# Kernel optimization log

Measured on AMD Instinct MI355X. Metric: run time of the kernel, lower is better.

Reference implementation:

```python
import jax, jax.numpy as jnp
import numpy as np
import math

NUM_HEADS = 8
HEAD_SIZE = 32

def get_alibi_slopes(n_heads):
    def pow2_slopes(n):
        start = 2.0 ** (-2.0 ** (-(math.log2(n) - 3)))
        ratio = start
        return [start * ratio ** i for i in range(n)]
    if math.log2(n_heads).is_integer():
        return np.array(pow2_slopes(n_heads), dtype=np.float32)
    cp2 = 2 ** math.floor(math.log2(n_heads))
    extra = pow2_slopes(2 * cp2)[0::2][: n_heads - cp2]
    return np.array(pow2_slopes(cp2) + extra, dtype=np.float32)

ALIBI_SLOPES = jnp.asarray(get_alibi_slopes(NUM_HEADS))  # [H]

def setup_inputs() -> dict:
    key = jax.random.key(0)
    ks = jax.random.split(key, 6)
    B, T, C = 32, 512, 256
    s = 1.0 / math.sqrt(C)
    return {
        "x": jax.random.normal(ks[0], (B, T, C), dtype=jnp.float32),
        "Wq": jax.random.normal(ks[1], (C, NUM_HEADS * HEAD_SIZE), dtype=jnp.float32) * s,
        "Wk": jax.random.normal(ks[2], (C, NUM_HEADS * HEAD_SIZE), dtype=jnp.float32) * s,
        "Wv": jax.random.normal(ks[3], (C, NUM_HEADS * HEAD_SIZE), dtype=jnp.float32) * s,
        "Wo": jax.random.normal(ks[4], (NUM_HEADS * HEAD_SIZE, C), dtype=jnp.float32) * s,
        "bo": jax.random.normal(ks[5], (C,), dtype=jnp.float32) * 0.01,
    }

def reference(x, Wq, Wk, Wv, Wo, bo):
    # Faithful eval-mode forward (dropout disabled) of the torch MultiHeadAttention.
    B, T, C = x.shape
    H, D = NUM_HEADS, HEAD_SIZE
    q = (x @ Wq).reshape(B, T, H, D).transpose(0, 2, 1, 3)  # [B,H,T,D]
    k = (x @ Wk).reshape(B, T, H, D).transpose(0, 2, 1, 3)
    v = (x @ Wv).reshape(B, T, H, D).transpose(0, 2, 1, 3)
    scale = 1.0 / math.sqrt(D)
    wei = jnp.einsum("bhtd,bhsd->bhts", q, k) * scale  # [B,H,T,T]
    pos = jnp.arange(T)
    rel = (pos[None, :] - pos[:, None]).astype(jnp.float32)  # bias[i,j] = j - i
    bias = ALIBI_SLOPES[:, None, None] * rel[None, :, :]      # [H,T,T]
    wei = wei + bias[None]
    causal = pos[None, :] <= pos[:, None]  # [T,T], True where j <= i
    wei = jnp.where(causal[None, None], wei, -jnp.inf)
    wei = jax.nn.softmax(wei, axis=-1)
    out = jnp.einsum("bhts,bhsd->bhtd", wei, v)  # [B,H,T,D]
    out = out.transpose(0, 2, 1, 3).reshape(B, T, H * D)
    return out @ Wo + bo
```

## Files before the change

kernel.cpp:

```cpp
#include <hip/hip_runtime.h>
#include <stdint.h>

#define LOG2E 1.4426950408889634f

typedef __attribute__((ext_vector_type(8))) short bf16x8;
typedef __attribute__((ext_vector_type(4))) float f32x4;

__device__ __forceinline__ unsigned short f2bf(float f) {
  union { float f; unsigned int u; } v; v.f = f;
  unsigned int u = v.u;
  u += 0x7FFFu + ((u >> 16) & 1u);
  return (unsigned short)(u >> 16);
}

__device__ __forceinline__ unsigned int cvt_pk_bf16(float lo, float hi) {
  unsigned int r;
  asm("v_cvt_pk_bf16_f32 %0, %1, %2" : "=v"(r) : "v"(lo), "v"(hi));
  return r;
}

struct WPtrs { const float* src[4]; unsigned short* dst[4]; };
__global__ void transpose_w(WPtrs p) {
  __shared__ float tile[32][33];
  const float* src = p.src[blockIdx.z];
  unsigned short* dst = p.dst[blockIdx.z];
  int x = blockIdx.x * 32 + threadIdx.x;
  int y = blockIdx.y * 32 + threadIdx.y;
  #pragma unroll
  for (int j = 0; j < 32; j += 8)
    tile[threadIdx.y + j][threadIdx.x] = src[(y + j) * 256 + x];
  __syncthreads();
  int xo = blockIdx.y * 32 + threadIdx.x;
  int yo = blockIdx.x * 32 + threadIdx.y;
  #pragma unroll
  for (int j = 0; j < 32; j += 8)
    dst[(yo + j) * 256 + xo] = f2bf(tile[threadIdx.x][threadIdx.y + j]);
}

__launch_bounds__(256, 3)
__global__ void gemm_qkv(const float* __restrict__ Ax,
                         const unsigned short* __restrict__ Wt,
                         unsigned short* __restrict__ q_out,
                         unsigned short* __restrict__ k_out,
                         unsigned short* __restrict__ vT) {
  __shared__ unsigned short As[64][72];
  __shared__ unsigned short Bs[256][72];
  const int tid = threadIdx.x;
  const int m0 = blockIdx.x * 64;
  const int wsel = blockIdx.y;
  const unsigned short* W = Wt + wsel * 65536;
  const int w = tid >> 6, lane = tid & 63;
  const int n0 = w * 64;
  const int lr = lane & 15, lg = lane >> 4;

  f32x4 acc[4][4] = {};

  for (int kt = 0; kt < 4; ++kt) {
    #pragma unroll
    for (int i = 0; i < 2; ++i) {
      int c = tid + i * 256;
      int row = c >> 3, colg = c & 7;
      const float* s = &Ax[(size_t)(m0 + row) * 256 + kt * 64 + colg * 8];
      float4 f0 = *reinterpret_cast<const float4*>(s);
      float4 f1 = *reinterpret_cast<const float4*>(s + 4);
      uint4 pk;
      pk.x = cvt_pk_bf16(f0.x, f0.y); pk.y = cvt_pk_bf16(f0.z, f0.w);
      pk.z = cvt_pk_bf16(f1.x, f1.y); pk.w = cvt_pk_bf16(f1.z, f1.w);
      *reinterpret_cast<uint4*>(&As[row][colg * 8]) = pk;
    }
    #pragma unroll
    for (int i = 0; i < 8; ++i) {
      int c = tid + i * 256;
      int row = c >> 3, colg = c & 7;
      *reinterpret_cast<int4*>(&Bs[row][colg * 8]) =
        *reinterpret_cast<const int4*>(&W[(size_t)row * 256 + kt * 64 + colg * 8]);
    }
    __syncthreads();
    #pragma unroll
    for (int kk = 0; kk < 2; ++kk) {
      bf16x8 af[4], bfr[4];
      #pragma unroll
      for (int mf = 0; mf < 4; ++mf)
        af[mf] = *reinterpret_cast<const bf16x8*>(&As[mf * 16 + lr][kk * 32 + lg * 8]);
      #pragma unroll
      for (int nf = 0; nf < 4; ++nf)
        bfr[nf] = *reinterpret_cast<const bf16x8*>(&Bs[n0 + nf * 16 + lr][kk * 32 + lg * 8]);
      #pragma unroll
      for (int mf = 0; mf < 4; ++mf)
        #pragma unroll
        for (int nf = 0; nf < 4; ++nf)
          acc[mf][nf] = __builtin_amdgcn_mfma_f32_16x16x32_bf16(af[mf], bfr[nf], acc[mf][nf], 0, 0, 0);
    }
    __syncthreads();
  }

  if (wsel < 2) {
    unsigned short* dst = (wsel == 0) ? q_out : k_out;
    #pragma unroll
    for (int mf = 0; mf < 4; ++mf)
      #pragma unroll
      for (int nf = 0; nf < 4; ++nf)
        #pragma unroll
        for (int r = 0; r < 4; ++r)
          dst[(size_t)(m0 + mf * 16 + lg * 4 + r) * 256 + (n0 + nf * 16 + lr)] =
            f2bf(acc[mf][nf][r]);
  } else {
    #pragma unroll
    for (int mf = 0; mf < 4; ++mf)
      #pragma unroll
      for (int nf = 0; nf < 4; ++nf) {
        int ncol = n0 + nf * 16 + lr;
        int h = ncol >> 5, d = ncol & 31;
        int m = m0 + mf * 16 + lg * 4;
        int b = m >> 9, t = m & 511;
        ushort4 pk;
        pk.x = f2bf(acc[mf][nf][0]); pk.y = f2bf(acc[mf][nf][1]);
        pk.z = f2bf(acc[mf][nf][2]); pk.w = f2bf(acc[mf][nf][3]);
        *reinterpret_cast<ushort4*>(&vT[((size_t)((b * 8 + h) * 32 + d)) * 512 + t]) = pk;
      }
  }
}

__launch_bounds__(256, 3)
__global__ void gemm_out(const unsigned short* __restrict__ Ab,
                         const unsigned short* __restrict__ W,
                         const float* __restrict__ bo,
                         float* __restrict__ f_out) {
  __shared__ unsigned short As[128][72];
  __shared__ unsigned short Bs[128][72];
  const int tid = threadIdx.x;
  const int m0 = blockIdx.x * 128;
  const int n0 = blockIdx.y * 128;
  const int w = tid >> 6, lane = tid & 63;
  const int wm = (w >> 1) * 64, wn = (w & 1) * 64;
  const int lr = lane & 15, lg = lane >> 4;

  f32x4 acc[4][4] = {};

  for (int kt = 0; kt < 4; ++kt) {
    #pragma unroll
    for (int cc = 0; cc < 4; ++cc) {
      int c = tid + cc * 256;
      int row = c >> 3, colg = c & 7;
      *reinterpret_cast<int4*>(&As[row][colg * 8]) =
        *reinterpret_cast<const int4*>(&Ab[(size_t)(m0 + row) * 256 + kt * 64 + colg * 8]);
      *reinterpret_cast<int4*>(&Bs[row][colg * 8]) =
        *reinterpret_cast<const int4*>(&W[(size_t)(n0 + row) * 256 + kt * 64 + colg * 8]);
    }
    __syncthreads();
    #pragma unroll
    for (int kk = 0; kk < 2; ++kk) {
      bf16x8 af[4], bfr[4];
      #pragma unroll
      for (int mf = 0; mf < 4; ++mf)
        af[mf] = *reinterpret_cast<const bf16x8*>(&As[wm + mf * 16 + lr][kk * 32 + lg * 8]);
      #pragma unroll
      for (int nf = 0; nf < 4; ++nf)
        bfr[nf] = *reinterpret_cast<const bf16x8*>(&Bs[wn + nf * 16 + lr][kk * 32 + lg * 8]);
      #pragma unroll
      for (int mf = 0; mf < 4; ++mf)
        #pragma unroll
        for (int nf = 0; nf < 4; ++nf)
          acc[mf][nf] = __builtin_amdgcn_mfma_f32_16x16x32_bf16(af[mf], bfr[nf], acc[mf][nf], 0, 0, 0);
    }
    __syncthreads();
  }

  #pragma unroll
  for (int mf = 0; mf < 4; ++mf)
    #pragma unroll
    for (int nf = 0; nf < 4; ++nf)
      #pragma unroll
      for (int r = 0; r < 4; ++r) {
        int ncol = n0 + wn + nf * 16 + lr;
        f_out[(size_t)(m0 + wm + mf * 16 + lg * 4 + r) * 256 + ncol] = acc[mf][nf][r] + bo[ncol];
      }
}

struct CSt {
  bf16x8 qf;
  f32x4 o0, o1;
  float m, l, bb0;
  int nfull, qq;
};

__device__ __forceinline__ void attn_init(CSt& st, int c, const unsigned short* qb,
    int b, int h, int lr, int lg, float slope2) {
  st.qq = c * 16;
  st.qf = *reinterpret_cast<const bf16x8*>(
      &qb[(size_t)(b * 512 + st.qq + lr) * 256 + h * 32 + lg * 8]);
  f32x4 z = {0.f, 0.f, 0.f, 0.f};
  st.o0 = z; st.o1 = z;
  st.m = -1e30f; st.l = 0.f;
  st.nfull = (st.qq >= 63) ? ((st.qq - 63) / 64 + 1) : 0;
  st.bb0 = slope2 * (float)(lg * 4 - lr - st.qq);
}

__device__ __forceinline__ void attn_step(CSt& st, int s,
    const bf16x8* kf, const bf16x8* vf, char* __restrict__ Pw,
    int lr, int lg, float scale2, float slope2, const float* cc, int swz) {
  const int kb0 = s * 64;
  f32x4 sv[4];
  #pragma unroll
  for (int t = 0; t < 4; ++t) {
    f32x4 z = {0.f, 0.f, 0.f, 0.f};
    sv[t] = __builtin_amdgcn_mfma_f32_16x16x32_bf16(kf[t], st.qf, z, 0, 0, 0);
  }
  float bb = st.bb0 + slope2 * (float)kb0;
  float x[16];
  #pragma unroll
  for (int t = 0; t < 4; ++t)
    #pragma unroll
    for (int r = 0; r < 4; ++r)
      x[t * 4 + r] = sv[t][r] * scale2 + (bb + cc[t * 4 + r]);
  if (s >= st.nfull) {
    int thr = st.qq + lr - kb0 - lg * 4;
    #pragma unroll
    for (int t = 0; t < 4; ++t)
      #pragma unroll
      for (int r = 0; r < 4; ++r)
        x[t * 4 + r] = ((t * 16 + r) <= thr) ? x[t * 4 + r] : -1e30f;
  }
  float bm = x[0];
  #pragma unroll
  for (int j = 1; j < 16; ++j) bm = fmaxf(bm, x[j]);
  bm = fmaxf(bm, __shfl_xor(bm, 16));
  bm = fmaxf(bm, __shfl_xor(bm, 32));
  float mn = fmaxf(st.m, bm);
  float alpha = __builtin_amdgcn_exp2f(st.m - mn);
  st.m = mn;
  st.l *= alpha;
  #pragma unroll
  for (int r = 0; r < 4; ++r) { st.o0[r] *= alpha; st.o1[r] *= alpha; }
  float ps = 0.f;
  #pragma unroll
  for (int j = 0; j < 16; ++j) { x[j] = __builtin_amdgcn_exp2f(x[j] - mn); ps += x[j]; }
  st.l += ps;
  char* Prow = Pw + lr * 128;
  #pragma unroll
  for (int t = 0; t < 4; ++t)
    #pragma unroll
    for (int pp = 0; pp < 2; ++pp) {
      unsigned int w2 = cvt_pk_bf16(x[t * 4 + 2 * pp], x[t * 4 + 2 * pp + 1]);
      *reinterpret_cast<unsigned int*>(Prow + ((t * 32 + lg * 8 + pp * 4) ^ swz)) = w2;
    }
  #pragma unroll
  for (int ks = 0; ks < 2; ++ks) {
    bf16x8 pb = *reinterpret_cast<const bf16x8*>(Prow + ((ks * 64 + lg * 16) ^ swz));
    st.o0 = __builtin_amdgcn_mfma_f32_16x16x32_bf16(vf[ks * 2 + 0], pb, st.o0, 0, 0, 0);
    st.o1 = __builtin_amdgcn_mfma_f32_16x16x32_bf16(vf[ks * 2 + 1], pb, st.o1, 0, 0, 0);
  }
}

__device__ __forceinline__ void attn_fin(CSt& st, unsigned short* __restrict__ ob,
                                         int b, int h, int lr, int lg) {
  float l = st.l;
  l += __shfl_xor(l, 16);
  l += __shfl_xor(l, 32);
  float inv = 1.0f / l;
  unsigned int w0 = cvt_pk_bf16(st.o0[0] * inv, st.o0[1] * inv);
  unsigned int w1 = cvt_pk_bf16(st.o0[2] * inv, st.o0[3] * inv);
  unsigned int w2 = cvt_pk_bf16(st.o1[0] * inv, st.o1[1] * inv);
  unsigned int w3 = cvt_pk_bf16(st.o1[2] * inv, st.o1[3] * inv);
  size_t obase = (size_t)(b * 512 + st.qq + lr) * 256 + h * 32;
  *reinterpret_cast<uint2*>(&ob[obase + lg * 4]) = make_uint2(w0, w1);
  *reinterpret_cast<uint2*>(&ob[obase + 16 + lg * 4]) = make_uint2(w2, w3);
}

__launch_bounds__(256, 2)
__global__ void attn_k(const unsigned short* __restrict__ qb,
                       const unsigned short* __restrict__ kb,
                       const unsigned short* __restrict__ vT,
                       unsigned short* __restrict__ ob) {
  __shared__ unsigned short Ks[512 * 32];
  __shared__ unsigned short Vs[32 * 512];
  __shared__ char Pb[16384];
  const int p = blockIdx.x, h = blockIdx.y, b = blockIdx.z;
  const int tid = threadIdx.x, wv = tid >> 6, lane = tid & 63;
  const int lr = lane & 15, lg = lane >> 4;

  {
    const unsigned short* ksrc = kb + ((size_t)b * 512) * 256 + h * 32;
    #pragma unroll
    for (int it = 0; it < 8; ++it) {
      int idx = tid + it * 256;
      int row = idx >> 2, g = idx & 3;
      int gs = g ^ ((row >> 1) & 3);
      *reinterpret_cast<int4*>(&Ks[row * 32 + gs * 8]) =
        *reinterpret_cast<const int4*>(&ksrc[(size_t)row * 256 + g * 8]);
    }
    const unsigned short* vsrc = vT + ((size_t)(b * 8 + h) * 32) * 512;
    #pragma unroll
    for (int it = 0; it < 8; ++it) {
      int idx = tid + it * 256;
      int d = idx >> 6, cg = idx & 63;
      int col = (cg * 8) ^ ((d & 7) << 3);
      *reinterpret_cast<int4*>(&Vs[d * 512 + col]) =
        *reinterpret_cast<const int4*>(&vsrc[(size_t)d * 512 + cg * 8]);
    }
  }
  __syncthreads();

  const float scale2 = 0.17677669529663687f * LOG2E;
  const float slope2 = exp2f(-(float)(h + 1)) * LOG2E;
  float cc[16];
  #pragma unroll
  for (int t = 0; t < 4; ++t)
    #pragma unroll
    for (int r = 0; r < 4; ++r) cc[t * 4 + r] = slope2 * (float)(t * 16 + r);
  const int swz = (lr & 7) << 4;
  const int kchunk = (lg ^ ((lr >> 1) & 3)) * 8;
  char* Pw0 = Pb + wv * 4096;
  char* Pw1 = Pw0 + 2048;

  const int g = p * 4 + wv;
  const int c0 = g, c1 = 15 - g, c2 = 16 + g, c3 = 31 - g;
  CSt s0, s1, s2, s3;
  attn_init(s0, c0, qb, b, h, lr, lg, slope2);
  attn_init(s1, c1, qb, b, h, lr, lg, slope2);
  attn_init(s2, c2, qb, b, h, lr, lg, slope2);
  attn_init(s3, c3, qb, b, h, lr, lg, slope2);
  const int n0 = c0 / 4 + 1, n1 = c1 / 4 + 1, n2 = c2 / 4 + 1, n3 = c3 / 4 + 1;

  for (int s = 0; s < n3; ++s) {
    const int kb0 = s * 64;
    bf16x8 kf[4], vf[4];
    #pragma unroll
    for (int t = 0; t < 4; ++t)
      kf[t] = *reinterpret_cast<const bf16x8*>(&Ks[(kb0 + t * 16 + lr) * 32 + kchunk]);
    #pragma unroll
    for (int ks = 0; ks < 2; ++ks)
      #pragma unroll
      for (int dt = 0; dt < 2; ++dt) {
        int d = dt * 16 + lr;
        int col = (kb0 + ks * 32 + lg * 8) ^ ((d & 7) << 3);
        vf[ks * 2 + dt] = *reinterpret_cast<const bf16x8*>(&Vs[d * 512 + col]);
      }
    if (s < n0) attn_step(s0, s, kf, vf, Pw0, lr, lg, scale2, slope2, cc, swz);
    if (s < n1) attn_step(s1, s, kf, vf, Pw1, lr, lg, scale2, slope2, cc, swz);
    if (s < n2) attn_step(s2, s, kf, vf, Pw0, lr, lg, scale2, slope2, cc, swz);
    attn_step(s3, s, kf, vf, Pw1, lr, lg, scale2, slope2, cc, swz);
  }

  attn_fin(s0, ob, b, h, lr, lg);
  attn_fin(s1, ob, b, h, lr, lg);
  attn_fin(s2, ob, b, h, lr, lg);
  attn_fin(s3, ob, b, h, lr, lg);
}

extern "C" void kernel_launch(void* const* d_in, const int* in_sizes, int n_in,
                              void* d_out, int out_size, void* d_ws, size_t ws_size,
                              hipStream_t stream) {
  const float* x  = (const float*)d_in[0];
  const float* Wq = (const float*)d_in[1];
  const float* Wk = (const float*)d_in[2];
  const float* Wv = (const float*)d_in[3];
  const float* Wo = (const float*)d_in[4];
  const float* bo = (const float*)d_in[5];
  float* out = (float*)d_out;

  char* ws = (char*)d_ws;
  unsigned short* qb = (unsigned short*)(ws);
  unsigned short* kb = (unsigned short*)(ws + (8u  << 20));
  unsigned short* vT = (unsigned short*)(ws + (16u << 20));
  unsigned short* ob = (unsigned short*)(ws + (24u << 20));
  unsigned short* wt = (unsigned short*)(ws + (32u << 20));

  WPtrs p;
  p.src[0] = Wq; p.src[1] = Wk; p.src[2] = Wv; p.src[3] = Wo;
  p.dst[0] = wt; p.dst[1] = wt + 65536; p.dst[2] = wt + 2 * 65536; p.dst[3] = wt + 3 * 65536;
  transpose_w<<<dim3(8, 8, 4), dim3(32, 8), 0, stream>>>(p);

  gemm_qkv<<<dim3(256, 3), 256, 0, stream>>>(x, wt, qb, kb, vT);
  attn_k<<<dim3(2, 8, 32), 256, 0, stream>>>(qb, kb, vT, ob);
  gemm_out<<<dim3(128, 2), 256, 0, stream>>>(ob, wt + 3 * 65536, bo, out);
}
```

Measured before the change: 58.70 us.

## Drop LDS staging in attention, read K/V from global and shuffle P in registers

The attention kernel stops staging K and V for the whole head in shared memory and instead loads the MFMA fragments straight from global memory (L2/L1-cached) on each step. The P tile is no longer written to and read back from LDS; packed bf16 values are moved between lanes with wave shuffles to form the MFMA B operand. Each wave now handles two balanced query chunks instead of four, the grid doubles, and launch bounds target 3 blocks per SM. This removes the upfront LDS fill, the block barrier and the LDS round-trip for P, at the cost of redundant global reads of K/V across blocks, uncoalesced strided fragment loads, and extra shuffle instructions.

```diff
diff --git a/kernel.cpp b/kernel.cpp
--- a/kernel.cpp
+++ b/kernel.cpp
@@ -197,8 +197,8 @@
 }
 
 __device__ __forceinline__ void attn_step(CSt& st, int s,
-    const bf16x8* kf, const bf16x8* vf, char* __restrict__ Pw,
-    int lr, int lg, float scale2, float slope2, const float* cc, int swz) {
+    const bf16x8* kf, const bf16x8* vf,
+    int lr, int lg, float scale2, float slope2, const float* cc) {
   const int kb0 = s * 64;
   f32x4 sv[4];
   #pragma unroll
@@ -236,19 +236,30 @@
   #pragma unroll
   for (int j = 0; j < 16; ++j) { x[j] = __builtin_amdgcn_exp2f(x[j] - mn); ps += x[j]; }
   st.l += ps;
-  char* Prow = Pw + lr * 128;
+  unsigned int wpk[4][2];
   #pragma unroll
   for (int t = 0; t < 4; ++t)
     #pragma unroll
-    for (int pp = 0; pp < 2; ++pp) {
-      unsigned int w2 = cvt_pk_bf16(x[t * 4 + 2 * pp], x[t * 4 + 2 * pp + 1]);
-      *reinterpret_cast<unsigned int*>(Prow + ((t * 32 + lg * 8 + pp * 4) ^ swz)) = w2;
-    }
+    for (int pp = 0; pp < 2; ++pp)
+      wpk[t][pp] = cvt_pk_bf16(x[t * 4 + 2 * pp], x[t * 4 + 2 * pp + 1]);
+  const int src0 = lr + (((lg & 1) * 2) << 4);
+  const int src1 = src0 + 16;
+  const bool hi = (lg >> 1) != 0;
   #pragma unroll
   for (int ks = 0; ks < 2; ++ks) {
-    bf16x8 pb = *reinterpret_cast<const bf16x8*>(Prow + ((ks * 64 + lg * 16) ^ swz));
-    st.o0 = __builtin_amdgcn_mfma_f32_16x16x32_bf16(vf[ks * 2 + 0], pb, st.o0, 0, 0, 0);
-    st.o1 = __builtin_amdgcn_mfma_f32_16x16x32_bf16(vf[ks * 2 + 1], pb, st.o1, 0, 0, 0);
+    unsigned long long Ap = ((unsigned long long)wpk[2 * ks + 1][0] << 32) | wpk[2 * ks][0];
+    unsigned long long Bp = ((unsigned long long)wpk[2 * ks + 1][1] << 32) | wpk[2 * ks][1];
+    unsigned long long A0 = (unsigned long long)__shfl((long long)Ap, src0, 64);
+    unsigned long long B0 = (unsigned long long)__shfl((long long)Bp, src0, 64);
+    unsigned long long A1 = (unsigned long long)__shfl((long long)Ap, src1, 64);
+    unsigned long long B1 = (unsigned long long)__shfl((long long)Bp, src1, 64);
+    union { uint4 u; bf16x8 v; } pb;
+    pb.u.x = hi ? (unsigned int)(A0 >> 32) : (unsigned int)A0;
+    pb.u.y = hi ? (unsigned int)(B0 >> 32) : (unsigned int)B0;
+    pb.u.z = hi ? (unsigned int)(A1 >> 32) : (unsigned int)A1;
+    pb.u.w = hi ? (unsigned int)(B1 >> 32) : (unsigned int)B1;
+    st.o0 = __builtin_amdgcn_mfma_f32_16x16x32_bf16(vf[ks * 2 + 0], pb.v, st.o0, 0, 0, 0);
+    st.o1 = __builtin_amdgcn_mfma_f32_16x16x32_bf16(vf[ks * 2 + 1], pb.v, st.o1, 0, 0, 0);
   }
 }
 
@@ -267,39 +278,14 @@
   *reinterpret_cast<uint2*>(&ob[obase + 16 + lg * 4]) = make_uint2(w2, w3);
 }
 
-__launch_bounds__(256, 2)
+__launch_bounds__(256, 3)
 __global__ void attn_k(const unsigned short* __restrict__ qb,
                        const unsigned short* __restrict__ kb,
                        const unsigned short* __restrict__ vT,
                        unsigned short* __restrict__ ob) {
-  __shared__ unsigned short Ks[512 * 32];
-  __shared__ unsigned short Vs[32 * 512];
-  __shared__ char Pb[16384];
-  const int p = blockIdx.x, h = blockIdx.y, b = blockIdx.z;
+  const int h = blockIdx.y, b = blockIdx.z;
   const int tid = threadIdx.x, wv = tid >> 6, lane = tid & 63;
   const int lr = lane & 15, lg = lane >> 4;
-
-  {
-    const unsigned short* ksrc = kb + ((size_t)b * 512) * 256 + h * 32;
-    #pragma unroll
-    for (int it = 0; it < 8; ++it) {
-      int idx = tid + it * 256;
-      int row = idx >> 2, g = idx & 3;
-      int gs = g ^ ((row >> 1) & 3);
-      *reinterpret_cast<int4*>(&Ks[row * 32 + gs * 8]) =
-        *reinterpret_cast<const int4*>(&ksrc[(size_t)row * 256 + g * 8]);
-    }
-    const unsigned short* vsrc = vT + ((size_t)(b * 8 + h) * 32) * 512;
-    #pragma unroll
-    for (int it = 0; it < 8; ++it) {
-      int idx = tid + it * 256;
-      int d = idx >> 6, cg = idx & 63;
-      int col = (cg * 8) ^ ((d & 7) << 3);
-      *reinterpret_cast<int4*>(&Vs[d * 512 + col]) =
-        *reinterpret_cast<const int4*>(&vsrc[(size_t)d * 512 + cg * 8]);
-    }
-  }
-  __syncthreads();
 
   const float scale2 = 0.17677669529663687f * LOG2E;
   const float slope2 = exp2f(-(float)(h + 1)) * LOG2E;
@@ -308,44 +294,36 @@
   for (int t = 0; t < 4; ++t)
     #pragma unroll
     for (int r = 0; r < 4; ++r) cc[t * 4 + r] = slope2 * (float)(t * 16 + r);
-  const int swz = (lr & 7) << 4;
-  const int kchunk = (lg ^ ((lr >> 1) & 3)) * 8;
-  char* Pw0 = Pb + wv * 4096;
-  char* Pw1 = Pw0 + 2048;
-
-  const int g = p * 4 + wv;
-  const int c0 = g, c1 = 15 - g, c2 = 16 + g, c3 = 31 - g;
-  CSt s0, s1, s2, s3;
-  attn_init(s0, c0, qb, b, h, lr, lg, slope2);
-  attn_init(s1, c1, qb, b, h, lr, lg, slope2);
-  attn_init(s2, c2, qb, b, h, lr, lg, slope2);
-  attn_init(s3, c3, qb, b, h, lr, lg, slope2);
-  const int n0 = c0 / 4 + 1, n1 = c1 / 4 + 1, n2 = c2 / 4 + 1, n3 = c3 / 4 + 1;
-
-  for (int s = 0; s < n3; ++s) {
+
+  const int j = blockIdx.x * 4 + wv;
+  const int cA = j, cB = 31 - j;
+  CSt A, B;
+  attn_init(A, cA, qb, b, h, lr, lg, slope2);
+  attn_init(B, cB, qb, b, h, lr, lg, slope2);
+  const int nA = cA / 4 + 1, nB = cB / 4 + 1;
+
+  const unsigned short* kbase = kb + ((size_t)b * 512) * 256 + h * 32;
+  const unsigned short* vbase = vT + ((size_t)(b * 8 + h) * 32) * 512;
+
+  for (int s = 0; s < nB; ++s) {
     const int kb0 = s * 64;
     bf16x8 kf[4], vf[4];
     #pragma unroll
     for (int t = 0; t < 4; ++t)
-      kf[t] = *reinterpret_cast<const bf16x8*>(&Ks[(kb0 + t * 16 + lr) * 32 + kchunk]);
+      kf[t] = *reinterpret_cast<const bf16x8*>(
+          &kbase[(size_t)(kb0 + t * 16 + lr) * 256 + lg * 8]);
     #pragma unroll
     for (int ks = 0; ks < 2; ++ks)
       #pragma unroll
-      for (int dt = 0; dt < 2; ++dt) {
-        int d = dt * 16 + lr;
-        int col = (kb0 + ks * 32 + lg * 8) ^ ((d & 7) << 3);
-        vf[ks * 2 + dt] = *reinterpret_cast<const bf16x8*>(&Vs[d * 512 + col]);
-      }
-    if (s < n0) attn_step(s0, s, kf, vf, Pw0, lr, lg, scale2, slope2, cc, swz);
-    if (s < n1) attn_step(s1, s, kf, vf, Pw1, lr, lg, scale2, slope2, cc, swz);
-    if (s < n2) attn_step(s2, s, kf, vf, Pw0, lr, lg, scale2, slope2, cc, swz);
-    attn_step(s3, s, kf, vf, Pw1, lr, lg, scale2, slope2, cc, swz);
-  }
-
-  attn_fin(s0, ob, b, h, lr, lg);
-  attn_fin(s1, ob, b, h, lr, lg);
-  attn_fin(s2, ob, b, h, lr, lg);
-  attn_fin(s3, ob, b, h, lr, lg);
+      for (int dt = 0; dt < 2; ++dt)
+        vf[ks * 2 + dt] = *reinterpret_cast<const bf16x8*>(
+            &vbase[(size_t)(dt * 16 + lr) * 512 + kb0 + ks * 32 + lg * 8]);
+    if (s < nA) attn_step(A, s, kf, vf, lr, lg, scale2, slope2, cc);
+    attn_step(B, s, kf, vf, lr, lg, scale2, slope2, cc);
+  }
+
+  attn_fin(A, ob, b, h, lr, lg);
+  attn_fin(B, ob, b, h, lr, lg);
 }
 
 extern "C" void kernel_launch(void* const* d_in, const int* in_sizes, int n_in,
@@ -372,6 +350,6 @@
   transpose_w<<<dim3(8, 8, 4), dim3(32, 8), 0, stream>>>(p);
 
   gemm_qkv<<<dim3(256, 3), 256, 0, stream>>>(x, wt, qb, kb, vT);
-  attn_k<<<dim3(2, 8, 32), 256, 0, stream>>>(qb, kb, vT, ob);
+  attn_k<<<dim3(4, 8, 32), 256, 0, stream>>>(qb, kb, vT, ob);
   gemm_out<<<dim3(128, 2), 256, 0, stream>>>(ob, wt + 3 * 65536, bo, out);
 }
```

Result: slower. 69.82 us (+18.9%).

## Halve per-wave chunks, read V from global, double attention grid

Applied to the files above, without the earlier changes.

The attention kernel now gives each wave two balanced query chunks (j and 31-j) instead of four. The grid doubles to 4x8x32 blocks and launch bounds rise to 4 blocks per CU. V is no longer staged in shared memory and is read directly from global memory (through the caches) every step, which cuts LDS use to raise occupancy. The trade-off is that each block reloads K, and V fragments now come from global/L2 with higher latency instead of from LDS.

```diff
diff --git a/kernel.cpp b/kernel.cpp
--- a/kernel.cpp
+++ b/kernel.cpp
@@ -267,14 +267,13 @@
   *reinterpret_cast<uint2*>(&ob[obase + 16 + lg * 4]) = make_uint2(w2, w3);
 }
 
-__launch_bounds__(256, 2)
+__launch_bounds__(256, 4)
 __global__ void attn_k(const unsigned short* __restrict__ qb,
                        const unsigned short* __restrict__ kb,
                        const unsigned short* __restrict__ vT,
                        unsigned short* __restrict__ ob) {
   __shared__ unsigned short Ks[512 * 32];
-  __shared__ unsigned short Vs[32 * 512];
-  __shared__ char Pb[16384];
+  __shared__ char Pb[8192];
   const int p = blockIdx.x, h = blockIdx.y, b = blockIdx.z;
   const int tid = threadIdx.x, wv = tid >> 6, lane = tid & 63;
   const int lr = lane & 15, lg = lane >> 4;
@@ -289,15 +288,6 @@
       *reinterpret_cast<int4*>(&Ks[row * 32 + gs * 8]) =
         *reinterpret_cast<const int4*>(&ksrc[(size_t)row * 256 + g * 8]);
     }
-    const unsigned short* vsrc = vT + ((size_t)(b * 8 + h) * 32) * 512;
-    #pragma unroll
-    for (int it = 0; it < 8; ++it) {
-      int idx = tid + it * 256;
-      int d = idx >> 6, cg = idx & 63;
-      int col = (cg * 8) ^ ((d & 7) << 3);
-      *reinterpret_cast<int4*>(&Vs[d * 512 + col]) =
-        *reinterpret_cast<const int4*>(&vsrc[(size_t)d * 512 + cg * 8]);
-    }
   }
   __syncthreads();
 
@@ -310,19 +300,18 @@
     for (int r = 0; r < 4; ++r) cc[t * 4 + r] = slope2 * (float)(t * 16 + r);
   const int swz = (lr & 7) << 4;
   const int kchunk = (lg ^ ((lr >> 1) & 3)) * 8;
-  char* Pw0 = Pb + wv * 4096;
-  char* Pw1 = Pw0 + 2048;
-
-  const int g = p * 4 + wv;
-  const int c0 = g, c1 = 15 - g, c2 = 16 + g, c3 = 31 - g;
-  CSt s0, s1, s2, s3;
-  attn_init(s0, c0, qb, b, h, lr, lg, slope2);
-  attn_init(s1, c1, qb, b, h, lr, lg, slope2);
-  attn_init(s2, c2, qb, b, h, lr, lg, slope2);
-  attn_init(s3, c3, qb, b, h, lr, lg, slope2);
-  const int n0 = c0 / 4 + 1, n1 = c1 / 4 + 1, n2 = c2 / 4 + 1, n3 = c3 / 4 + 1;
-
-  for (int s = 0; s < n3; ++s) {
+  char* Pw = Pb + wv * 2048;
+
+  const int j = p * 4 + wv;
+  const int cA = j, cB = 31 - j;
+  CSt A, B;
+  attn_init(A, cA, qb, b, h, lr, lg, slope2);
+  attn_init(B, cB, qb, b, h, lr, lg, slope2);
+  const int nA = cA / 4 + 1, nB = cB / 4 + 1;
+
+  const unsigned short* vbase = vT + ((size_t)(b * 8 + h) * 32) * 512;
+
+  for (int s = 0; s < nB; ++s) {
     const int kb0 = s * 64;
     bf16x8 kf[4], vf[4];
     #pragma unroll
@@ -331,21 +320,15 @@
     #pragma unroll
     for (int ks = 0; ks < 2; ++ks)
       #pragma unroll
-      for (int dt = 0; dt < 2; ++dt) {
-        int d = dt * 16 + lr;
-        int col = (kb0 + ks * 32 + lg * 8) ^ ((d & 7) << 3);
-        vf[ks * 2 + dt] = *reinterpret_cast<const bf16x8*>(&Vs[d * 512 + col]);
-      }
-    if (s < n0) attn_step(s0, s, kf, vf, Pw0, lr, lg, scale2, slope2, cc, swz);
-    if (s < n1) attn_step(s1, s, kf, vf, Pw1, lr, lg, scale2, slope2, cc, swz);
-    if (s < n2) attn_step(s2, s, kf, vf, Pw0, lr, lg, scale2, slope2, cc, swz);
-    attn_step(s3, s, kf, vf, Pw1, lr, lg, scale2, slope2, cc, swz);
-  }
-
-  attn_fin(s0, ob, b, h, lr, lg);
-  attn_fin(s1, ob, b, h, lr, lg);
-  attn_fin(s2, ob, b, h, lr, lg);
-  attn_fin(s3, ob, b, h, lr, lg);
+      for (int dt = 0; dt < 2; ++dt)
+        vf[ks * 2 + dt] = *reinterpret_cast<const bf16x8*>(
+            &vbase[(size_t)(dt * 16 + lr) * 512 + kb0 + ks * 32 + lg * 8]);
+    if (s < nA) attn_step(A, s, kf, vf, Pw, lr, lg, scale2, slope2, cc, swz);
+    attn_step(B, s, kf, vf, Pw, lr, lg, scale2, slope2, cc, swz);
+  }
+
+  attn_fin(A, ob, b, h, lr, lg);
+  attn_fin(B, ob, b, h, lr, lg);
 }
 
 extern "C" void kernel_launch(void* const* d_in, const int* in_sizes, int n_in,
@@ -372,6 +355,6 @@
   transpose_w<<<dim3(8, 8, 4), dim3(32, 8), 0, stream>>>(p);
 
   gemm_qkv<<<dim3(256, 3), 256, 0, stream>>>(x, wt, qb, kb, vT);
-  attn_k<<<dim3(2, 8, 32), 256, 0, stream>>>(qb, kb, vT, ob);
+  attn_k<<<dim3(4, 8, 32), 256, 0, stream>>>(qb, kb, vT, ob);
   gemm_out<<<dim3(128, 2), 256, 0, stream>>>(ob, wt + 3 * 65536, bo, out);
 }
```

New measurement: 64.13 us. +9.2%, slower.

## Fold softmax scale into Q, process two key blocks per step, add MFMA priority hints

Applied to the files above, without the earlier changes.

Folds the 1/sqrt(D)*log2e softmax scale into the Q projection epilogue, which removes a per-score multiply in the attention inner loop. The attention loop now advances two 64-key blocks at a time: one online-softmax rescale covers 128 keys and only the last block is masked. MFMA sections are wrapped in s_setprio to favour matrix issue across waves. The price is more live registers (kf/vf doubled, 32-wide score arrays), which may pressure occupancy under launch_bounds(256,2), and the P buffer is now shared by all four chunks of a wave.

```diff
diff --git a/kernel.cpp b/kernel.cpp
--- a/kernel.cpp
+++ b/kernel.cpp
@@ -2,6 +2,7 @@
 #include <stdint.h>
 
 #define LOG2E 1.4426950408889634f
+#define QSCALE_LN2 0.25506068f
 
 typedef __attribute__((ext_vector_type(8))) short bf16x8;
 typedef __attribute__((ext_vector_type(4))) float f32x4;
@@ -96,6 +97,7 @@
 
   if (wsel < 2) {
     unsigned short* dst = (wsel == 0) ? q_out : k_out;
+    const float qs = (wsel == 0) ? QSCALE_LN2 : 1.0f;
     #pragma unroll
     for (int mf = 0; mf < 4; ++mf)
       #pragma unroll
@@ -103,7 +105,7 @@
         #pragma unroll
         for (int r = 0; r < 4; ++r)
           dst[(size_t)(m0 + mf * 16 + lg * 4 + r) * 256 + (n0 + nf * 16 + lr)] =
-            f2bf(acc[mf][nf][r]);
+            f2bf(acc[mf][nf][r] * qs);
   } else {
     #pragma unroll
     for (int mf = 0; mf < 4; ++mf)
@@ -198,21 +200,23 @@
 
 __device__ __forceinline__ void attn_step(CSt& st, int s,
     const bf16x8* kf, const bf16x8* vf, char* __restrict__ Pw,
-    int lr, int lg, float scale2, float slope2, const float* cc, int swz) {
+    int lr, int lg, float slope2, const float* cc, int swz) {
   const int kb0 = s * 64;
   f32x4 sv[4];
+  __builtin_amdgcn_s_setprio(1);
   #pragma unroll
   for (int t = 0; t < 4; ++t) {
     f32x4 z = {0.f, 0.f, 0.f, 0.f};
     sv[t] = __builtin_amdgcn_mfma_f32_16x16x32_bf16(kf[t], st.qf, z, 0, 0, 0);
   }
+  __builtin_amdgcn_s_setprio(0);
   float bb = st.bb0 + slope2 * (float)kb0;
   float x[16];
   #pragma unroll
   for (int t = 0; t < 4; ++t)
     #pragma unroll
     for (int r = 0; r < 4; ++r)
-      x[t * 4 + r] = sv[t][r] * scale2 + (bb + cc[t * 4 + r]);
+      x[t * 4 + r] = sv[t][r] + (bb + cc[t * 4 + r]);
   if (s >= st.nfull) {
     int thr = st.qq + lr - kb0 - lg * 4;
     #pragma unroll
@@ -236,7 +240,7 @@
   #pragma unroll
   for (int j = 0; j < 16; ++j) { x[j] = __builtin_amdgcn_exp2f(x[j] - mn); ps += x[j]; }
   st.l += ps;
-  char* Prow = Pw + lr * 128;
+  char* Prow = Pw + lr * 256;
   #pragma unroll
   for (int t = 0; t < 4; ++t)
     #pragma unroll
@@ -244,12 +248,81 @@
       unsigned int w2 = cvt_pk_bf16(x[t * 4 + 2 * pp], x[t * 4 + 2 * pp + 1]);
       *reinterpret_cast<unsigned int*>(Prow + ((t * 32 + lg * 8 + pp * 4) ^ swz)) = w2;
     }
+  __builtin_amdgcn_s_setprio(1);
   #pragma unroll
   for (int ks = 0; ks < 2; ++ks) {
     bf16x8 pb = *reinterpret_cast<const bf16x8*>(Prow + ((ks * 64 + lg * 16) ^ swz));
     st.o0 = __builtin_amdgcn_mfma_f32_16x16x32_bf16(vf[ks * 2 + 0], pb, st.o0, 0, 0, 0);
     st.o1 = __builtin_amdgcn_mfma_f32_16x16x32_bf16(vf[ks * 2 + 1], pb, st.o1, 0, 0, 0);
   }
+  __builtin_amdgcn_s_setprio(0);
+}
+
+__device__ __forceinline__ void attn_step2(CSt& st, int s, bool maskB,
+    const bf16x8* kf, const bf16x8* vf, char* __restrict__ Pw,
+    int lr, int lg, float slope2, const float* cc, int swz) {
+  const int kb0 = s * 64;
+  f32x4 sv[8];
+  __builtin_amdgcn_s_setprio(1);
+  #pragma unroll
+  for (int t = 0; t < 8; ++t) {
+    f32x4 z = {0.f, 0.f, 0.f, 0.f};
+    sv[t] = __builtin_amdgcn_mfma_f32_16x16x32_bf16(kf[t], st.qf, z, 0, 0, 0);
+  }
+  __builtin_amdgcn_s_setprio(0);
+  const float bbA = st.bb0 + slope2 * (float)kb0;
+  const float bbB = bbA + slope2 * 64.0f;
+  float x[32];
+  #pragma unroll
+  for (int t = 0; t < 4; ++t)
+    #pragma unroll
+    for (int r = 0; r < 4; ++r) {
+      x[t * 4 + r]      = sv[t][r]     + (bbA + cc[t * 4 + r]);
+      x[16 + t * 4 + r] = sv[4 + t][r] + (bbB + cc[t * 4 + r]);
+    }
+  if (maskB) {
+    int thr = st.qq + lr - (kb0 + 64) - lg * 4;
+    #pragma unroll
+    for (int t = 0; t < 4; ++t)
+      #pragma unroll
+      for (int r = 0; r < 4; ++r)
+        x[16 + t * 4 + r] = ((t * 16 + r) <= thr) ? x[16 + t * 4 + r] : -1e30f;
+  }
+  float bm = x[0];
+  #pragma unroll
+  for (int j = 1; j < 32; ++j) bm = fmaxf(bm, x[j]);
+  bm = fmaxf(bm, __shfl_xor(bm, 16));
+  bm = fmaxf(bm, __shfl_xor(bm, 32));
+  float mn = fmaxf(st.m, bm);
+  float alpha = __builtin_amdgcn_exp2f(st.m - mn);
+  st.m = mn;
+  st.l *= alpha;
+  #pragma unroll
+  for (int r = 0; r < 4; ++r) { st.o0[r] *= alpha; st.o1[r] *= alpha; }
+  float ps = 0.f;
+  #pragma unroll
+  for (int j = 0; j < 32; ++j) { x[j] = __builtin_amdgcn_exp2f(x[j] - mn); ps += x[j]; }
+  st.l += ps;
+  char* Prow = Pw + lr * 256;
+  #pragma unroll
+  for (int t = 0; t < 4; ++t)
+    #pragma unroll
+    for (int pp = 0; pp < 2; ++pp) {
+      const int cb = (t * 32 + lg * 8 + pp * 4) ^ swz;
+      *reinterpret_cast<unsigned int*>(Prow + cb) =
+          cvt_pk_bf16(x[t * 4 + 2 * pp], x[t * 4 + 2 * pp + 1]);
+      *reinterpret_cast<unsigned int*>(Prow + 128 + cb) =
+          cvt_pk_bf16(x[16 + t * 4 + 2 * pp], x[16 + t * 4 + 2 * pp + 1]);
+    }
+  __builtin_amdgcn_s_setprio(1);
+  #pragma unroll
+  for (int ks = 0; ks < 4; ++ks) {
+    const int cb = (ks >> 1) * 128 + ((((ks & 1) * 64) + lg * 16) ^ swz);
+    bf16x8 pb = *reinterpret_cast<const bf16x8*>(Prow + cb);
+    st.o0 = __builtin_amdgcn_mfma_f32_16x16x32_bf16(vf[ks * 2 + 0], pb, st.o0, 0, 0, 0);
+    st.o1 = __builtin_amdgcn_mfma_f32_16x16x32_bf16(vf[ks * 2 + 1], pb, st.o1, 0, 0, 0);
+  }
+  __builtin_amdgcn_s_setprio(0);
 }
 
 __device__ __forceinline__ void attn_fin(CSt& st, unsigned short* __restrict__ ob,
@@ -267,6 +340,16 @@
   *reinterpret_cast<uint2*>(&ob[obase + 16 + lg * 4]) = make_uint2(w2, w3);
 }
 
+__device__ __forceinline__ void chunk_phase(CSt& st, int s, int nc,
+    const bf16x8* kf, const bf16x8* vf, char* Pw,
+    int lr, int lg, float slope2, const float* cc, int swz) {
+  if (s >= nc) return;
+  if (s + 1 < nc)
+    attn_step2(st, s, (s + 2 >= nc), kf, vf, Pw, lr, lg, slope2, cc, swz);
+  else
+    attn_step(st, s, kf, vf, Pw, lr, lg, slope2, cc, swz);
+}
+
 __launch_bounds__(256, 2)
 __global__ void attn_k(const unsigned short* __restrict__ qb,
                        const unsigned short* __restrict__ kb,
@@ -301,7 +384,6 @@
   }
   __syncthreads();
 
-  const float scale2 = 0.17677669529663687f * LOG2E;
   const float slope2 = exp2f(-(float)(h + 1)) * LOG2E;
   float cc[16];
   #pragma unroll
@@ -310,8 +392,7 @@
     for (int r = 0; r < 4; ++r) cc[t * 4 + r] = slope2 * (float)(t * 16 + r);
   const int swz = (lr & 7) << 4;
   const int kchunk = (lg ^ ((lr >> 1) & 3)) * 8;
-  char* Pw0 = Pb + wv * 4096;
-  char* Pw1 = Pw0 + 2048;
+  char* Pw = Pb + wv * 4096;
 
   const int g = p * 4 + wv;
   const int c0 = g, c1 = 15 - g, c2 = 16 + g, c3 = 31 - g;
@@ -322,24 +403,24 @@
   attn_init(s3, c3, qb, b, h, lr, lg, slope2);
   const int n0 = c0 / 4 + 1, n1 = c1 / 4 + 1, n2 = c2 / 4 + 1, n3 = c3 / 4 + 1;
 
-  for (int s = 0; s < n3; ++s) {
+  for (int s = 0; s < n3; s += 2) {
     const int kb0 = s * 64;
-    bf16x8 kf[4], vf[4];
-    #pragma unroll
-    for (int t = 0; t < 4; ++t)
+    bf16x8 kf[8], vf[8];
+    #pragma unroll
+    for (int t = 0; t < 8; ++t)
       kf[t] = *reinterpret_cast<const bf16x8*>(&Ks[(kb0 + t * 16 + lr) * 32 + kchunk]);
     #pragma unroll
-    for (int ks = 0; ks < 2; ++ks)
+    for (int ks = 0; ks < 4; ++ks)
       #pragma unroll
       for (int dt = 0; dt < 2; ++dt) {
         int d = dt * 16 + lr;
         int col = (kb0 + ks * 32 + lg * 8) ^ ((d & 7) << 3);
         vf[ks * 2 + dt] = *reinterpret_cast<const bf16x8*>(&Vs[d * 512 + col]);
       }
-    if (s < n0) attn_step(s0, s, kf, vf, Pw0, lr, lg, scale2, slope2, cc, swz);
-    if (s < n1) attn_step(s1, s, kf, vf, Pw1, lr, lg, scale2, slope2, cc, swz);
-    if (s < n2) attn_step(s2, s, kf, vf, Pw0, lr, lg, scale2, slope2, cc, swz);
-    attn_step(s3, s, kf, vf, Pw1, lr, lg, scale2, slope2, cc, swz);
+    chunk_phase(s0, s, n0, kf, vf, Pw, lr, lg, slope2, cc, swz);
+    chunk_phase(s1, s, n1, kf, vf, Pw, lr, lg, slope2, cc, swz);
+    chunk_phase(s2, s, n2, kf, vf, Pw, lr, lg, slope2, cc, swz);
+    chunk_phase(s3, s, n3, kf, vf, Pw, lr, lg, slope2, cc, swz);
   }
 
   attn_fin(s0, ob, b, h, lr, lg);
```

Measured after the change: 57.28 us, median of 2. 1.02x faster.
